# Optimization experiments

Hardware: AMD Instinct MI355X
Metric: run time of the kernel (lower is better)

Reference implementation:

```python
import jax, jax.numpy as jnp
import numpy as np

EMBED = 1024
HEADS = 16
HEAD_DIM = EMBED // HEADS


def setup_inputs() -> dict:
    key = jax.random.key(0)
    ks = jax.random.split(key, 9)
    N, L = 2, 2048
    values = jax.random.normal(ks[0], (N, L, EMBED), dtype=jnp.float32)
    keys = jax.random.normal(ks[1], (N, L, EMBED), dtype=jnp.float32)
    query = jax.random.normal(ks[2], (N, L, EMBED), dtype=jnp.float32)
    mask = jax.random.randint(ks[3], (N, 1, L, L), 0, 2, dtype=jnp.int32)
    s = 1.0 / np.sqrt(HEAD_DIM)
    Wv = jax.random.normal(ks[4], (HEAD_DIM, HEAD_DIM), dtype=jnp.float32) * s
    Wk = jax.random.normal(ks[5], (HEAD_DIM, HEAD_DIM), dtype=jnp.float32) * s
    Wq = jax.random.normal(ks[6], (HEAD_DIM, HEAD_DIM), dtype=jnp.float32) * s
    Wout = jax.random.normal(ks[7], (EMBED, EMBED), dtype=jnp.float32) * (1.0 / np.sqrt(EMBED))
    bout = jax.random.normal(ks[8], (EMBED,), dtype=jnp.float32) * 0.01
    return {"values": values, "keys": keys, "query": query, "mask": mask,
            "Wv": Wv, "Wk": Wk, "Wq": Wq, "Wout": Wout, "bout": bout}


def reference(values, keys, query, mask, Wv, Wk, Wq, Wout, bout):
    N, Lq, _ = query.shape
    Lk = keys.shape[1]
    # split heads: [N, L, H, D]
    v = values.reshape(N, Lk, HEADS, HEAD_DIM)
    k = keys.reshape(N, Lk, HEADS, HEAD_DIM)
    q = query.reshape(N, Lq, HEADS, HEAD_DIM)
    # per-head Linear (weight shared across heads), torch Linear: x @ W.T
    v = jnp.einsum('nlhd,ed->nlhe', v, Wv)
    k = jnp.einsum('nlhd,ed->nlhe', k, Wk)
    q = jnp.einsum('nlhd,ed->nlhe', q, Wq)
    # scores [N, H, Q, K]
    scores = jnp.einsum('nqhd,nkhd->nhqk', q, k)
    scores = jnp.where(mask == 0, jnp.float32(-1e20), scores)
    # NOTE: original scales by sqrt(embed_size), not sqrt(head_dim)
    attn = jax.nn.softmax(scores / jnp.sqrt(jnp.float32(EMBED)), axis=3)
    out = jnp.einsum('nhqk,nkhd->nqhd', attn, v).reshape(N, Lq, EMBED)
    return out @ Wout.T + bout
```

## Files before the change

kernel.cpp:

```cpp
#include <hip/hip_runtime.h>
#include <hip/hip_bf16.h>
#include <stdint.h>

typedef unsigned short u16;
typedef __attribute__((ext_vector_type(8))) short short8;
typedef __attribute__((ext_vector_type(4))) float float4_;

#define N_B   2
#define L_SEQ 2048
#define H_N   16
#define D_H   64
#define EMB   1024
#define KWORDS (L_SEQ/64)

#define C2 0.045084220027780106f

#define KP_OFF 0u
#define VP_OFF (8u*1024u*1024u)
#define X2_OFF (16u*1024u*1024u)
#define MP_OFF (24u*1024u*1024u)
#define WB_OFF (25u*1024u*1024u)

#define PREP_MASK  32768u
#define PREP_CVTW  (PREP_MASK + 512u)
#define PREP_PROJK (PREP_CVTW + 1024u)
#define PREP_TOTAL (PREP_PROJK + 1024u)

__device__ __forceinline__ u16 f2bf(float f) {
    __hip_bfloat16 h = __float2bfloat16(f);
    return *reinterpret_cast<u16*>(&h);
}
__device__ __forceinline__ short8 load8f(const float* p) {
    float4_ a = *(const float4_*)p;
    float4_ b = *(const float4_*)(p + 4);
    short8 r;
    r[0] = (short)f2bf(a[0]); r[1] = (short)f2bf(a[1]);
    r[2] = (short)f2bf(a[2]); r[3] = (short)f2bf(a[3]);
    r[4] = (short)f2bf(b[0]); r[5] = (short)f2bf(b[1]);
    r[6] = (short)f2bf(b[2]); r[7] = (short)f2bf(b[3]);
    return r;
}
__device__ __forceinline__ void gload16(const void* g, void* l) {
    __builtin_amdgcn_global_load_lds(
        (const __attribute__((address_space(1))) uint32_t*)(size_t)g,
        (__attribute__((address_space(3))) uint32_t*)(size_t)l, 16, 0, 0);
}
__device__ __forceinline__ uint32_t cvtpk(float a, float b) {
    uint32_t r;
    asm("v_cvt_pk_bf16_f32 %0, %1, %2" : "=v"(r) : "v"(a), "v"(b));
    return r;
}

__global__ __launch_bounds__(256) void prep_kernel(const int* __restrict__ mask,
                                                   unsigned long long* __restrict__ mp,
                                                   const float* __restrict__ Wout,
                                                   u16* __restrict__ wb,
                                                   const float* __restrict__ keys,
                                                   const float* __restrict__ Wk,
                                                   u16* __restrict__ kp,
                                                   const float* __restrict__ values,
                                                   const float* __restrict__ Wv,
                                                   u16* __restrict__ vpT) {
    unsigned bid = blockIdx.x;
    int tid = threadIdx.x;

    if (bid < PREP_MASK) {
        int wid  = (bid * 256 + tid) >> 6;
        int lane = tid & 63;
        int m = mask[(size_t)wid * 64 + lane];
        unsigned long long bits = __ballot(m != 0);
        if (lane == 0) mp[wid] = bits;
        return;
    }
    if (bid < PREP_CVTW) {
        int i = ((bid - PREP_MASK) * 256 + tid) * 8;
        *(short8*)(wb + i) = load8f(Wout + i);
        return;
    }

    bool isK = bid < PREP_PROJK;
    unsigned lb = bid - (isK ? PREP_CVTW : PREP_PROJK);
    const float* x = isK ? keys : values;
    const float* W = isK ? Wk : Wv;

    int lt = lb & 31;
    int h  = (lb >> 5) & 15;
    int n  = lb >> 9;
    int w = tid >> 6, lane = tid & 63;
    int g = lane >> 4, r16 = lane & 15;
    int l0 = lt * 64 + w * 16;

    const float* xrow = x + ((size_t)(n * L_SEQ + l0 + r16)) * EMB + h * 64;
    short8 a0 = load8f(xrow + 8 * g);
    short8 a1 = load8f(xrow + 32 + 8 * g);

    short8 wf[4][2];
    for (int eb = 0; eb < 4; eb++)
        for (int ch = 0; ch < 2; ch++)
            wf[eb][ch] = load8f(W + (eb * 16 + r16) * 64 + ch * 32 + 8 * g);

    if (isK) {
        u16* ob = kp + ((size_t)((n * H_N + h) * L_SEQ + l0)) * 64;
        for (int eb = 0; eb < 4; eb++) {
            float4_ c = {0.f, 0.f, 0.f, 0.f};
            c = __builtin_amdgcn_mfma_f32_16x16x32_bf16(a0, wf[eb][0], c, 0, 0, 0);
            c = __builtin_amdgcn_mfma_f32_16x16x32_bf16(a1, wf[eb][1], c, 0, 0, 0);
            for (int i = 0; i < 4; i++)
                ob[(size_t)(4 * g + i) * 64 + eb * 16 + r16] = f2bf(c[i]);
        }
    } else {
        u16* obase = vpT + ((size_t)(n * H_N + h)) * (64 * L_SEQ) + l0 + r16;
        for (int eb = 0; eb < 4; eb++) {
            float4_ c = {0.f, 0.f, 0.f, 0.f};
            c = __builtin_amdgcn_mfma_f32_16x16x32_bf16(wf[eb][0], a0, c, 0, 0, 0);
            c = __builtin_amdgcn_mfma_f32_16x16x32_bf16(wf[eb][1], a1, c, 0, 0, 0);
            for (int i = 0; i < 4; i++)
                obase[(size_t)(eb * 16 + 4 * g + i) * L_SEQ] = f2bf(c[i]);
        }
    }
}

__global__ __launch_bounds__(256) void attn_kernel(const float* __restrict__ query,
                                                   const float* __restrict__ Wq,
                                                   const u16* __restrict__ kp,
                                                   const u16* __restrict__ vpT,
                                                   const unsigned long long* __restrict__ mp,
                                                   u16* __restrict__ x2) {
    __shared__ __align__(16) u16 Ks[64 * 64];
    __shared__ __align__(16) u16 Vt[64 * 64];
    __shared__ __align__(16) u16 Pt[4][2][16 * 64];

    int bid = blockIdx.x;
    int nh = bid & 31, qt = bid >> 5;
    int n = nh >> 4;
    int h = nh & 15;
    int tid = threadIdx.x;
    int w = tid >> 6, lane = tid & 63;
    int g = lane >> 4, r16 = lane & 15;
    int q0 = qt * 128 + w * 16;

    const u16* kb  = kp  + ((size_t)nh * L_SEQ) * 64;
    const u16* vtb = vpT + ((size_t)nh) * (64 * L_SEQ);

    int psw = (r16 & 7) << 4;

    short8 wf[4][2];
    for (int eb = 0; eb < 4; eb++)
        for (int ch = 0; ch < 2; ch++)
            wf[eb][ch] = load8f(Wq + (eb * 16 + r16) * 64 + ch * 32 + 8 * g);

    for (int s = 0; s < 2; s++) {
        const float* qrow = query + ((size_t)(n * L_SEQ + q0 + s * 64 + r16)) * EMB + h * 64;
        short8 a0 = load8f(qrow + 8 * g);
        short8 a1 = load8f(qrow + 32 + 8 * g);
        for (int eb = 0; eb < 4; eb++) {
            float4_ c = {0.f, 0.f, 0.f, 0.f};
            c = __builtin_amdgcn_mfma_f32_16x16x32_bf16(a0, wf[eb][0], c, 0, 0, 0);
            c = __builtin_amdgcn_mfma_f32_16x16x32_bf16(a1, wf[eb][1], c, 0, 0, 0);
            for (int i = 0; i < 4; i++) {
                int row = 4 * g + i;
                *(u16*)((char*)Pt[w][s] + row * 128 + (((eb * 16 + r16) * 2) ^ ((row & 7) << 4))) = f2bf(c[i] * C2);
            }
        }
    }
    short8 aq00 = *(const short8*)((char*)Pt[w][0] + r16 * 128 + ((16 * g) ^ psw));
    short8 aq01 = *(const short8*)((char*)Pt[w][0] + r16 * 128 + ((64 + 16 * g) ^ psw));
    short8 aq10 = *(const short8*)((char*)Pt[w][1] + r16 * 128 + ((16 * g) ^ psw));
    short8 aq11 = *(const short8*)((char*)Pt[w][1] + r16 * 128 + ((64 + 16 * g) ^ psw));

    float4_ o0[4] = {}, o1[4] = {};
    float lp0 = 0.f, lp1 = 0.f;
    const unsigned long long* mprow0 = mp + ((size_t)n * L_SEQ + q0 + r16) * KWORDS;
    const unsigned long long* mprow1 = mprow0 + (size_t)64 * KWORDS;

    int rs = (w << 3) + (lane >> 3);
    int cc = (lane & 7) ^ ((lane >> 3) & 7);
    char* ldsK0 = (char*)Ks + w * 1024;
    char* ldsV0 = (char*)Vt + w * 1024;

    for (int kt = 0; kt < 32; kt++) {
        int k0 = kt * 64;
        __syncthreads();
        for (int h2 = 0; h2 < 2; h2++) {
            int r = rs + 32 * h2;
            gload16(kb  + (size_t)(k0 + r) * 64 + cc * 8, ldsK0 + h2 * 4096);
            gload16(vtb + (size_t)r * L_SEQ + k0 + cc * 8, ldsV0 + h2 * 4096);
        }
        __syncthreads();

        unsigned long long word0 = mprow0[kt];
        unsigned long long word1 = mprow1[kt];

        for (int cb = 0; cb < 4; cb++) {
            int row = cb * 16 + r16;
            int sw = (row & 7) << 4;
            short8 bk0 = *(const short8*)((char*)Ks + row * 128 + ((16 * g) ^ sw));
            short8 bk1 = *(const short8*)((char*)Ks + row * 128 + ((64 + 16 * g) ^ sw));
            float4_ c0 = {0.f, 0.f, 0.f, 0.f};
            c0 = __builtin_amdgcn_mfma_f32_16x16x32_bf16(bk0, aq00, c0, 0, 0, 0);
            c0 = __builtin_amdgcn_mfma_f32_16x16x32_bf16(bk1, aq01, c0, 0, 0, 0);
            float4_ c1 = {0.f, 0.f, 0.f, 0.f};
            c1 = __builtin_amdgcn_mfma_f32_16x16x32_bf16(bk0, aq10, c1, 0, 0, 0);
            c1 = __builtin_amdgcn_mfma_f32_16x16x32_bf16(bk1, aq11, c1, 0, 0, 0);

            uint32_t nib0 = (uint32_t)(word0 >> (16 * cb + 4 * g)) & 0xFu;
            uint32_t nib1 = (uint32_t)(word1 >> (16 * cb + 4 * g)) & 0xFu;

            float p0 = (nib0 & 1u) ? exp2f(c0[0]) : 0.f;
            float p1 = (nib0 & 2u) ? exp2f(c0[1]) : 0.f;
            float p2 = (nib0 & 4u) ? exp2f(c0[2]) : 0.f;
            float p3 = (nib0 & 8u) ? exp2f(c0[3]) : 0.f;
            lp0 += (p0 + p1) + (p2 + p3);
            uint2 pk0; pk0.x = cvtpk(p0, p1); pk0.y = cvtpk(p2, p3);
            *(uint2*)((char*)Pt[w][0] + r16 * 128 + ((cb * 32 + 8 * g) ^ psw)) = pk0;

            float q0v = (nib1 & 1u) ? exp2f(c1[0]) : 0.f;
            float q1v = (nib1 & 2u) ? exp2f(c1[1]) : 0.f;
            float q2v = (nib1 & 4u) ? exp2f(c1[2]) : 0.f;
            float q3v = (nib1 & 8u) ? exp2f(c1[3]) : 0.f;
            lp1 += (q0v + q1v) + (q2v + q3v);
            uint2 pk1; pk1.x = cvtpk(q0v, q1v); pk1.y = cvtpk(q2v, q3v);
            *(uint2*)((char*)Pt[w][1] + r16 * 128 + ((cb * 32 + 8 * g) ^ psw)) = pk1;
        }

        short8 pb00 = *(const short8*)((char*)Pt[w][0] + r16 * 128 + ((16 * g) ^ psw));
        short8 pb01 = *(const short8*)((char*)Pt[w][0] + r16 * 128 + ((64 + 16 * g) ^ psw));
        short8 pb10 = *(const short8*)((char*)Pt[w][1] + r16 * 128 + ((16 * g) ^ psw));
        short8 pb11 = *(const short8*)((char*)Pt[w][1] + r16 * 128 + ((64 + 16 * g) ^ psw));

        for (int db = 0; db < 4; db++) {
            int row = db * 16 + r16;
            int sw = (row & 7) << 4;
            short8 av0 = *(const short8*)((char*)Vt + row * 128 + ((16 * g) ^ sw));
            short8 av1 = *(const short8*)((char*)Vt + row * 128 + ((64 + 16 * g) ^ sw));
            o0[db] = __builtin_amdgcn_mfma_f32_16x16x32_bf16(av0, pb00, o0[db], 0, 0, 0);
            o0[db] = __builtin_amdgcn_mfma_f32_16x16x32_bf16(av1, pb01, o0[db], 0, 0, 0);
            o1[db] = __builtin_amdgcn_mfma_f32_16x16x32_bf16(av0, pb10, o1[db], 0, 0, 0);
            o1[db] = __builtin_amdgcn_mfma_f32_16x16x32_bf16(av1, pb11, o1[db], 0, 0, 0);
        }
    }

    float t0 = lp0;
    t0 += __shfl_xor(t0, 16);
    t0 += __shfl_xor(t0, 32);
    float inv0 = 1.f / fmaxf(t0, 1e-30f);
    float t1 = lp1;
    t1 += __shfl_xor(t1, 16);
    t1 += __shfl_xor(t1, 32);
    float inv1 = 1.f / fmaxf(t1, 1e-30f);

    u16* ob0 = x2 + ((size_t)(n * L_SEQ + q0 + r16)) * EMB + h * 64;
    u16* ob1 = x2 + ((size_t)(n * L_SEQ + q0 + 64 + r16)) * EMB + h * 64;
    for (int db = 0; db < 4; db++)
        for (int i = 0; i < 4; i++) {
            ob0[db * 16 + 4 * g + i] = f2bf(o0[db][i] * inv0);
            ob1[db * 16 + 4 * g + i] = f2bf(o1[db][i] * inv1);
        }
}

__global__ __launch_bounds__(512) void outgemm_kernel(const u16* __restrict__ x2,
                                                      const u16* __restrict__ Wb,
                                                      const float* __restrict__ bout,
                                                      float* __restrict__ out) {
    __shared__ __align__(16) u16 As[128 * 64];
    __shared__ __align__(16) u16 Bs[128 * 64];

    int bid = blockIdx.x;
    int mt = bid >> 3, nt = bid & 7;
    int m0 = mt * 128, n0 = nt * 128;
    int tid = threadIdx.x;
    int w = tid >> 6, lane = tid & 63;
    int g = lane >> 4, r16 = lane & 15;
    int wr = w >> 2, wc = w & 3;

    float4_ acc[4][2] = {};

    int rs = (w << 3) + (lane >> 3);
    int cc = (lane & 7) ^ ((lane >> 3) & 7);
    char* ldsA0 = (char*)As + w * 1024;
    char* ldsB0 = (char*)Bs + w * 1024;

    for (int kbk = 0; kbk < 16; kbk++) {
        int kk0 = kbk * 64;
        __syncthreads();
        for (int h2 = 0; h2 < 2; h2++) {
            int r = rs + 64 * h2;
            gload16(x2 + (size_t)(m0 + r) * EMB + kk0 + cc * 8, ldsA0 + h2 * 8192);
            gload16(Wb + (size_t)(n0 + r) * EMB + kk0 + cc * 8, ldsB0 + h2 * 8192);
        }
        __syncthreads();

        short8 afr[4][2], bfr[2][2];
        for (int sm = 0; sm < 4; sm++)
            for (int ch = 0; ch < 2; ch++) {
                int row = wr * 64 + sm * 16 + r16;
                afr[sm][ch] = *(const short8*)((char*)As + row * 128 + ((ch * 64 + 16 * g) ^ ((row & 7) << 4)));
            }
        for (int sn = 0; sn < 2; sn++)
            for (int ch = 0; ch < 2; ch++) {
                int row = wc * 32 + sn * 16 + r16;
                bfr[sn][ch] = *(const short8*)((char*)Bs + row * 128 + ((ch * 64 + 16 * g) ^ ((row & 7) << 4)));
            }
        for (int sm = 0; sm < 4; sm++)
            for (int sn = 0; sn < 2; sn++) {
                acc[sm][sn] = __builtin_amdgcn_mfma_f32_16x16x32_bf16(afr[sm][0], bfr[sn][0], acc[sm][sn], 0, 0, 0);
                acc[sm][sn] = __builtin_amdgcn_mfma_f32_16x16x32_bf16(afr[sm][1], bfr[sn][1], acc[sm][sn], 0, 0, 0);
            }
    }

    for (int sm = 0; sm < 4; sm++)
        for (int sn = 0; sn < 2; sn++) {
            int nn = n0 + wc * 32 + sn * 16 + r16;
            float bv = bout[nn];
            for (int i = 0; i < 4; i++) {
                int mm = m0 + wr * 64 + sm * 16 + 4 * g + i;
                out[(size_t)mm * EMB + nn] = acc[sm][sn][i] + bv;
            }
        }
}

extern "C" void kernel_launch(void* const* d_in, const int* in_sizes, int n_in,
                              void* d_out, int out_size, void* d_ws, size_t ws_size,
                              hipStream_t stream) {
    const float* values = (const float*)d_in[0];
    const float* keys   = (const float*)d_in[1];
    const float* query  = (const float*)d_in[2];
    const int*   mask   = (const int*)d_in[3];
    const float* Wv     = (const float*)d_in[4];
    const float* Wk     = (const float*)d_in[5];
    const float* Wq     = (const float*)d_in[6];
    const float* Wout   = (const float*)d_in[7];
    const float* bout   = (const float*)d_in[8];
    float* out = (float*)d_out;

    char* ws = (char*)d_ws;
    u16* kp  = (u16*)(ws + KP_OFF);
    u16* vpT = (u16*)(ws + VP_OFF);
    u16* x2  = (u16*)(ws + X2_OFF);
    unsigned long long* mpk = (unsigned long long*)(ws + MP_OFF);
    u16* wb  = (u16*)(ws + WB_OFF);

    prep_kernel<<<PREP_TOTAL, 256, 0, stream>>>(mask, mpk, Wout, wb,
                                                keys, Wk, kp, values, Wv, vpT);
    attn_kernel<<<512, 256, 0, stream>>>(query, Wq, kp, vpT, mpk, x2);
    outgemm_kernel<<<256, 512, 0, stream>>>(x2, wb, bout, out);
}
```

Baseline: 252.4 us.

## Double-buffer K/V tiles in attention, halve query tile, coarsen mask packing

```diff
diff --git a/kernel.cpp b/kernel.cpp
--- a/kernel.cpp
+++ b/kernel.cpp
@@ -21,7 +21,7 @@
 #define MP_OFF (24u*1024u*1024u)
 #define WB_OFF (25u*1024u*1024u)
 
-#define PREP_MASK  32768u
+#define PREP_MASK  2048u
 #define PREP_CVTW  (PREP_MASK + 512u)
 #define PREP_PROJK (PREP_CVTW + 1024u)
 #define PREP_TOTAL (PREP_PROJK + 1024u)
@@ -48,6 +48,11 @@
 __device__ __forceinline__ uint32_t cvtpk(float a, float b) {
     uint32_t r;
     asm("v_cvt_pk_bf16_f32 %0, %1, %2" : "=v"(r) : "v"(a), "v"(b));
+    return r;
+}
+__device__ __forceinline__ float fexp2(float x) {
+    float r;
+    asm("v_exp_f32 %0, %1" : "=v"(r) : "v"(x));
     return r;
 }
 
@@ -65,11 +70,14 @@
     int tid = threadIdx.x;
 
     if (bid < PREP_MASK) {
-        int wid  = (bid * 256 + tid) >> 6;
         int lane = tid & 63;
-        int m = mask[(size_t)wid * 64 + lane];
-        unsigned long long bits = __ballot(m != 0);
-        if (lane == 0) mp[wid] = bits;
+        int wv   = tid >> 6;
+        for (int j = 0; j < 16; j++) {
+            int wid = bid * 64 + j * 4 + wv;
+            int m = mask[(size_t)wid * 64 + lane];
+            unsigned long long bits = __ballot(m != 0);
+            if (lane == 0) mp[wid] = bits;
+        }
         return;
     }
     if (bid < PREP_CVTW) {
@@ -126,9 +134,9 @@
                                                    const u16* __restrict__ vpT,
                                                    const unsigned long long* __restrict__ mp,
                                                    u16* __restrict__ x2) {
-    __shared__ __align__(16) u16 Ks[64 * 64];
-    __shared__ __align__(16) u16 Vt[64 * 64];
-    __shared__ __align__(16) u16 Pt[4][2][16 * 64];
+    __shared__ __align__(16) u16 Ks[2][64 * 64];
+    __shared__ __align__(16) u16 Vt[2][64 * 64];
+    __shared__ __align__(16) u16 Pt[4][16 * 64];
 
     int bid = blockIdx.x;
     int nh = bid & 31, qt = bid >> 5;
@@ -137,125 +145,116 @@
     int tid = threadIdx.x;
     int w = tid >> 6, lane = tid & 63;
     int g = lane >> 4, r16 = lane & 15;
-    int q0 = qt * 128 + w * 16;
+    int q0 = qt * 64 + w * 16;
 
     const u16* kb  = kp  + ((size_t)nh * L_SEQ) * 64;
     const u16* vtb = vpT + ((size_t)nh) * (64 * L_SEQ);
 
     int psw = (r16 & 7) << 4;
 
-    short8 wf[4][2];
-    for (int eb = 0; eb < 4; eb++)
-        for (int ch = 0; ch < 2; ch++)
-            wf[eb][ch] = load8f(Wq + (eb * 16 + r16) * 64 + ch * 32 + 8 * g);
-
-    for (int s = 0; s < 2; s++) {
-        const float* qrow = query + ((size_t)(n * L_SEQ + q0 + s * 64 + r16)) * EMB + h * 64;
+    {
+        const float* qrow = query + ((size_t)(n * L_SEQ + q0 + r16)) * EMB + h * 64;
         short8 a0 = load8f(qrow + 8 * g);
         short8 a1 = load8f(qrow + 32 + 8 * g);
         for (int eb = 0; eb < 4; eb++) {
+            short8 w0 = load8f(Wq + (eb * 16 + r16) * 64 + 8 * g);
+            short8 w1 = load8f(Wq + (eb * 16 + r16) * 64 + 32 + 8 * g);
             float4_ c = {0.f, 0.f, 0.f, 0.f};
-            c = __builtin_amdgcn_mfma_f32_16x16x32_bf16(a0, wf[eb][0], c, 0, 0, 0);
-            c = __builtin_amdgcn_mfma_f32_16x16x32_bf16(a1, wf[eb][1], c, 0, 0, 0);
+            c = __builtin_amdgcn_mfma_f32_16x16x32_bf16(a0, w0, c, 0, 0, 0);
+            c = __builtin_amdgcn_mfma_f32_16x16x32_bf16(a1, w1, c, 0, 0, 0);
             for (int i = 0; i < 4; i++) {
                 int row = 4 * g + i;
-                *(u16*)((char*)Pt[w][s] + row * 128 + (((eb * 16 + r16) * 2) ^ ((row & 7) << 4))) = f2bf(c[i] * C2);
-            }
-        }
-    }
-    short8 aq00 = *(const short8*)((char*)Pt[w][0] + r16 * 128 + ((16 * g) ^ psw));
-    short8 aq01 = *(const short8*)((char*)Pt[w][0] + r16 * 128 + ((64 + 16 * g) ^ psw));
-    short8 aq10 = *(const short8*)((char*)Pt[w][1] + r16 * 128 + ((16 * g) ^ psw));
-    short8 aq11 = *(const short8*)((char*)Pt[w][1] + r16 * 128 + ((64 + 16 * g) ^ psw));
-
-    float4_ o0[4] = {}, o1[4] = {};
-    float lp0 = 0.f, lp1 = 0.f;
-    const unsigned long long* mprow0 = mp + ((size_t)n * L_SEQ + q0 + r16) * KWORDS;
-    const unsigned long long* mprow1 = mprow0 + (size_t)64 * KWORDS;
+                *(u16*)((char*)Pt[w] + row * 128 + (((eb * 16 + r16) * 2) ^ ((row & 7) << 4))) = f2bf(c[i] * C2);
+            }
+        }
+    }
+    short8 aq0 = *(const short8*)((char*)Pt[w] + r16 * 128 + ((16 * g) ^ psw));
+    short8 aq1 = *(const short8*)((char*)Pt[w] + r16 * 128 + ((64 + 16 * g) ^ psw));
+
+    float4_ o[4] = {};
+    float lpart = 0.f;
+    const unsigned long long* mprow = mp + ((size_t)n * L_SEQ + q0 + r16) * KWORDS;
 
     int rs = (w << 3) + (lane >> 3);
     int cc = (lane & 7) ^ ((lane >> 3) & 7);
-    char* ldsK0 = (char*)Ks + w * 1024;
-    char* ldsV0 = (char*)Vt + w * 1024;
+
+    #define STAGE(kt_, b_) do {                                                  \
+        int k0_ = (kt_) * 64;                                                    \
+        for (int h2 = 0; h2 < 2; h2++) {                                         \
+            int r_ = rs + 32 * h2;                                               \
+            gload16(kb  + (size_t)(k0_ + r_) * 64 + cc * 8,                      \
+                    (char*)Ks[b_] + w * 1024 + h2 * 4096);                       \
+            gload16(vtb + (size_t)r_ * L_SEQ + k0_ + cc * 8,                     \
+                    (char*)Vt[b_] + w * 1024 + h2 * 4096);                       \
+        }                                                                        \
+    } while (0)
+
+    STAGE(0, 0);
+    int cur = 0;
 
     for (int kt = 0; kt < 32; kt++) {
-        int k0 = kt * 64;
-        __syncthreads();
-        for (int h2 = 0; h2 < 2; h2++) {
-            int r = rs + 32 * h2;
-            gload16(kb  + (size_t)(k0 + r) * 64 + cc * 8, ldsK0 + h2 * 4096);
-            gload16(vtb + (size_t)r * L_SEQ + k0 + cc * 8, ldsV0 + h2 * 4096);
-        }
-        __syncthreads();
-
-        unsigned long long word0 = mprow0[kt];
-        unsigned long long word1 = mprow1[kt];
-
+        if (kt < 31) {
+            STAGE(kt + 1, cur ^ 1);
+            asm volatile("s_waitcnt vmcnt(4)" ::: "memory");
+        } else {
+            asm volatile("s_waitcnt vmcnt(0)" ::: "memory");
+        }
+        __builtin_amdgcn_sched_barrier(0);
+        __builtin_amdgcn_s_barrier();
+        __builtin_amdgcn_sched_barrier(0);
+
+        unsigned long long word = mprow[kt];
+        const char* ksb = (const char*)Ks[cur];
+        const char* vtbuf = (const char*)Vt[cur];
+
+        __builtin_amdgcn_s_setprio(1);
         for (int cb = 0; cb < 4; cb++) {
             int row = cb * 16 + r16;
             int sw = (row & 7) << 4;
-            short8 bk0 = *(const short8*)((char*)Ks + row * 128 + ((16 * g) ^ sw));
-            short8 bk1 = *(const short8*)((char*)Ks + row * 128 + ((64 + 16 * g) ^ sw));
-            float4_ c0 = {0.f, 0.f, 0.f, 0.f};
-            c0 = __builtin_amdgcn_mfma_f32_16x16x32_bf16(bk0, aq00, c0, 0, 0, 0);
-            c0 = __builtin_amdgcn_mfma_f32_16x16x32_bf16(bk1, aq01, c0, 0, 0, 0);
-            float4_ c1 = {0.f, 0.f, 0.f, 0.f};
-            c1 = __builtin_amdgcn_mfma_f32_16x16x32_bf16(bk0, aq10, c1, 0, 0, 0);
-            c1 = __builtin_amdgcn_mfma_f32_16x16x32_bf16(bk1, aq11, c1, 0, 0, 0);
-
-            uint32_t nib0 = (uint32_t)(word0 >> (16 * cb + 4 * g)) & 0xFu;
-            uint32_t nib1 = (uint32_t)(word1 >> (16 * cb + 4 * g)) & 0xFu;
-
-            float p0 = (nib0 & 1u) ? exp2f(c0[0]) : 0.f;
-            float p1 = (nib0 & 2u) ? exp2f(c0[1]) : 0.f;
-            float p2 = (nib0 & 4u) ? exp2f(c0[2]) : 0.f;
-            float p3 = (nib0 & 8u) ? exp2f(c0[3]) : 0.f;
-            lp0 += (p0 + p1) + (p2 + p3);
-            uint2 pk0; pk0.x = cvtpk(p0, p1); pk0.y = cvtpk(p2, p3);
-            *(uint2*)((char*)Pt[w][0] + r16 * 128 + ((cb * 32 + 8 * g) ^ psw)) = pk0;
-
-            float q0v = (nib1 & 1u) ? exp2f(c1[0]) : 0.f;
-            float q1v = (nib1 & 2u) ? exp2f(c1[1]) : 0.f;
-            float q2v = (nib1 & 4u) ? exp2f(c1[2]) : 0.f;
-            float q3v = (nib1 & 8u) ? exp2f(c1[3]) : 0.f;
-            lp1 += (q0v + q1v) + (q2v + q3v);
-            uint2 pk1; pk1.x = cvtpk(q0v, q1v); pk1.y = cvtpk(q2v, q3v);
-            *(uint2*)((char*)Pt[w][1] + r16 * 128 + ((cb * 32 + 8 * g) ^ psw)) = pk1;
-        }
-
-        short8 pb00 = *(const short8*)((char*)Pt[w][0] + r16 * 128 + ((16 * g) ^ psw));
-        short8 pb01 = *(const short8*)((char*)Pt[w][0] + r16 * 128 + ((64 + 16 * g) ^ psw));
-        short8 pb10 = *(const short8*)((char*)Pt[w][1] + r16 * 128 + ((16 * g) ^ psw));
-        short8 pb11 = *(const short8*)((char*)Pt[w][1] + r16 * 128 + ((64 + 16 * g) ^ psw));
+            short8 bk0 = *(const short8*)(ksb + row * 128 + ((16 * g) ^ sw));
+            short8 bk1 = *(const short8*)(ksb + row * 128 + ((64 + 16 * g) ^ sw));
+            float4_ c = {0.f, 0.f, 0.f, 0.f};
+            c = __builtin_amdgcn_mfma_f32_16x16x32_bf16(bk0, aq0, c, 0, 0, 0);
+            c = __builtin_amdgcn_mfma_f32_16x16x32_bf16(bk1, aq1, c, 0, 0, 0);
+
+            uint32_t nib = (uint32_t)(word >> (16 * cb + 4 * g)) & 0xFu;
+            float p0 = (nib & 1u) ? fexp2(c[0]) : 0.f;
+            float p1 = (nib & 2u) ? fexp2(c[1]) : 0.f;
+            float p2 = (nib & 4u) ? fexp2(c[2]) : 0.f;
+            float p3 = (nib & 8u) ? fexp2(c[3]) : 0.f;
+            lpart += (p0 + p1) + (p2 + p3);
+            uint2 pkv; pkv.x = cvtpk(p0, p1); pkv.y = cvtpk(p2, p3);
+            *(uint2*)((char*)Pt[w] + r16 * 128 + ((cb * 32 + 8 * g) ^ psw)) = pkv;
+        }
+
+        short8 pb0 = *(const short8*)((char*)Pt[w] + r16 * 128 + ((16 * g) ^ psw));
+        short8 pb1 = *(const short8*)((char*)Pt[w] + r16 * 128 + ((64 + 16 * g) ^ psw));
 
         for (int db = 0; db < 4; db++) {
             int row = db * 16 + r16;
             int sw = (row & 7) << 4;
-            short8 av0 = *(const short8*)((char*)Vt + row * 128 + ((16 * g) ^ sw));
-            short8 av1 = *(const short8*)((char*)Vt + row * 128 + ((64 + 16 * g) ^ sw));
-            o0[db] = __builtin_amdgcn_mfma_f32_16x16x32_bf16(av0, pb00, o0[db], 0, 0, 0);
-            o0[db] = __builtin_amdgcn_mfma_f32_16x16x32_bf16(av1, pb01, o0[db], 0, 0, 0);
-            o1[db] = __builtin_amdgcn_mfma_f32_16x16x32_bf16(av0, pb10, o1[db], 0, 0, 0);
-            o1[db] = __builtin_amdgcn_mfma_f32_16x16x32_bf16(av1, pb11, o1[db], 0, 0, 0);
-        }
-    }
-
-    float t0 = lp0;
-    t0 += __shfl_xor(t0, 16);
-    t0 += __shfl_xor(t0, 32);
-    float inv0 = 1.f / fmaxf(t0, 1e-30f);
-    float t1 = lp1;
-    t1 += __shfl_xor(t1, 16);
-    t1 += __shfl_xor(t1, 32);
-    float inv1 = 1.f / fmaxf(t1, 1e-30f);
-
-    u16* ob0 = x2 + ((size_t)(n * L_SEQ + q0 + r16)) * EMB + h * 64;
-    u16* ob1 = x2 + ((size_t)(n * L_SEQ + q0 + 64 + r16)) * EMB + h * 64;
+            short8 av0 = *(const short8*)(vtbuf + row * 128 + ((16 * g) ^ sw));
+            short8 av1 = *(const short8*)(vtbuf + row * 128 + ((64 + 16 * g) ^ sw));
+            o[db] = __builtin_amdgcn_mfma_f32_16x16x32_bf16(av0, pb0, o[db], 0, 0, 0);
+            o[db] = __builtin_amdgcn_mfma_f32_16x16x32_bf16(av1, pb1, o[db], 0, 0, 0);
+        }
+        __builtin_amdgcn_s_setprio(0);
+
+        __builtin_amdgcn_sched_barrier(0);
+        __builtin_amdgcn_s_barrier();
+        cur ^= 1;
+    }
+    #undef STAGE
+
+    float tot = lpart;
+    tot += __shfl_xor(tot, 16);
+    tot += __shfl_xor(tot, 32);
+    float inv = 1.f / fmaxf(tot, 1e-30f);
+
+    u16* ob = x2 + ((size_t)(n * L_SEQ + q0 + r16)) * EMB + h * 64;
     for (int db = 0; db < 4; db++)
-        for (int i = 0; i < 4; i++) {
-            ob0[db * 16 + 4 * g + i] = f2bf(o0[db][i] * inv0);
-            ob1[db * 16 + 4 * g + i] = f2bf(o1[db][i] * inv1);
-        }
+        for (int i = 0; i < 4; i++)
+            ob[db * 16 + 4 * g + i] = f2bf(o[db][i] * inv);
 }
 
 __global__ __launch_bounds__(512) void outgemm_kernel(const u16* __restrict__ x2,
@@ -342,6 +341,6 @@
 
     prep_kernel<<<PREP_TOTAL, 256, 0, stream>>>(mask, mpk, Wout, wb,
                                                 keys, Wk, kp, values, Wv, vpT);
-    attn_kernel<<<512, 256, 0, stream>>>(query, Wq, kp, vpT, mpk, x2);
+    attn_kernel<<<1024, 256, 0, stream>>>(query, Wq, kp, vpT, mpk, x2);
     outgemm_kernel<<<256, 512, 0, stream>>>(x2, wb, bout, out);
 }
```

After: 232.6 us. -7.8%, faster.

## Double-buffer LDS tiles in attention and output GEMM, use raw exp2, coarsen mask packing

Applied to the files above, without the earlier changes.

```diff
diff --git a/kernel.cpp b/kernel.cpp
--- a/kernel.cpp
+++ b/kernel.cpp
@@ -21,7 +21,7 @@
 #define MP_OFF (24u*1024u*1024u)
 #define WB_OFF (25u*1024u*1024u)
 
-#define PREP_MASK  32768u
+#define PREP_MASK  2048u
 #define PREP_CVTW  (PREP_MASK + 512u)
 #define PREP_PROJK (PREP_CVTW + 1024u)
 #define PREP_TOTAL (PREP_PROJK + 1024u)
@@ -48,6 +48,11 @@
 __device__ __forceinline__ uint32_t cvtpk(float a, float b) {
     uint32_t r;
     asm("v_cvt_pk_bf16_f32 %0, %1, %2" : "=v"(r) : "v"(a), "v"(b));
+    return r;
+}
+__device__ __forceinline__ float fexp2(float x) {
+    float r;
+    asm("v_exp_f32 %0, %1" : "=v"(r) : "v"(x));
     return r;
 }
 
@@ -65,11 +70,14 @@
     int tid = threadIdx.x;
 
     if (bid < PREP_MASK) {
-        int wid  = (bid * 256 + tid) >> 6;
         int lane = tid & 63;
-        int m = mask[(size_t)wid * 64 + lane];
-        unsigned long long bits = __ballot(m != 0);
-        if (lane == 0) mp[wid] = bits;
+        int wv   = tid >> 6;
+        for (int j = 0; j < 16; j++) {
+            int wid = bid * 64 + j * 4 + wv;
+            int m = mask[(size_t)wid * 64 + lane];
+            unsigned long long bits = __ballot(m != 0);
+            if (lane == 0) mp[wid] = bits;
+        }
         return;
     }
     if (bid < PREP_CVTW) {
@@ -126,8 +134,8 @@
                                                    const u16* __restrict__ vpT,
                                                    const unsigned long long* __restrict__ mp,
                                                    u16* __restrict__ x2) {
-    __shared__ __align__(16) u16 Ks[64 * 64];
-    __shared__ __align__(16) u16 Vt[64 * 64];
+    __shared__ __align__(16) u16 Ks[2][64 * 64];
+    __shared__ __align__(16) u16 Vt[2][64 * 64];
     __shared__ __align__(16) u16 Pt[4][2][16 * 64];
 
     int bid = blockIdx.x;
@@ -143,6 +151,22 @@
     const u16* vtb = vpT + ((size_t)nh) * (64 * L_SEQ);
 
     int psw = (r16 & 7) << 4;
+
+    int rs = (w << 3) + (lane >> 3);
+    int cc = (lane & 7) ^ ((lane >> 3) & 7);
+
+    #define STAGE(kt_, b_) do {                                                  \
+        int k0_ = (kt_) * 64;                                                    \
+        for (int h2 = 0; h2 < 2; h2++) {                                         \
+            int r_ = rs + 32 * h2;                                               \
+            gload16(kb  + (size_t)(k0_ + r_) * 64 + cc * 8,                      \
+                    (char*)Ks[b_] + w * 1024 + h2 * 4096);                       \
+            gload16(vtb + (size_t)r_ * L_SEQ + k0_ + cc * 8,                     \
+                    (char*)Vt[b_] + w * 1024 + h2 * 4096);                       \
+        }                                                                        \
+    } while (0)
+
+    STAGE(0, 0);
 
     short8 wf[4][2];
     for (int eb = 0; eb < 4; eb++)
@@ -173,29 +197,30 @@
     const unsigned long long* mprow0 = mp + ((size_t)n * L_SEQ + q0 + r16) * KWORDS;
     const unsigned long long* mprow1 = mprow0 + (size_t)64 * KWORDS;
 
-    int rs = (w << 3) + (lane >> 3);
-    int cc = (lane & 7) ^ ((lane >> 3) & 7);
-    char* ldsK0 = (char*)Ks + w * 1024;
-    char* ldsV0 = (char*)Vt + w * 1024;
-
+    int cur = 0;
     for (int kt = 0; kt < 32; kt++) {
-        int k0 = kt * 64;
-        __syncthreads();
-        for (int h2 = 0; h2 < 2; h2++) {
-            int r = rs + 32 * h2;
-            gload16(kb  + (size_t)(k0 + r) * 64 + cc * 8, ldsK0 + h2 * 4096);
-            gload16(vtb + (size_t)r * L_SEQ + k0 + cc * 8, ldsV0 + h2 * 4096);
-        }
-        __syncthreads();
-
         unsigned long long word0 = mprow0[kt];
         unsigned long long word1 = mprow1[kt];
-
+        __builtin_amdgcn_sched_barrier(0);
+        if (kt < 31) {
+            STAGE(kt + 1, cur ^ 1);
+            __builtin_amdgcn_sched_barrier(0);
+            asm volatile("s_waitcnt vmcnt(6)" ::: "memory");
+        } else {
+            asm volatile("s_waitcnt vmcnt(0)" ::: "memory");
+        }
+        __builtin_amdgcn_s_barrier();
+        __builtin_amdgcn_sched_barrier(0);
+
+        const char* ksb   = (const char*)Ks[cur];
+        const char* vtbuf = (const char*)Vt[cur];
+
+        __builtin_amdgcn_s_setprio(1);
         for (int cb = 0; cb < 4; cb++) {
             int row = cb * 16 + r16;
             int sw = (row & 7) << 4;
-            short8 bk0 = *(const short8*)((char*)Ks + row * 128 + ((16 * g) ^ sw));
-            short8 bk1 = *(const short8*)((char*)Ks + row * 128 + ((64 + 16 * g) ^ sw));
+            short8 bk0 = *(const short8*)(ksb + row * 128 + ((16 * g) ^ sw));
+            short8 bk1 = *(const short8*)(ksb + row * 128 + ((64 + 16 * g) ^ sw));
             float4_ c0 = {0.f, 0.f, 0.f, 0.f};
             c0 = __builtin_amdgcn_mfma_f32_16x16x32_bf16(bk0, aq00, c0, 0, 0, 0);
             c0 = __builtin_amdgcn_mfma_f32_16x16x32_bf16(bk1, aq01, c0, 0, 0, 0);
@@ -206,18 +231,18 @@
             uint32_t nib0 = (uint32_t)(word0 >> (16 * cb + 4 * g)) & 0xFu;
             uint32_t nib1 = (uint32_t)(word1 >> (16 * cb + 4 * g)) & 0xFu;
 
-            float p0 = (nib0 & 1u) ? exp2f(c0[0]) : 0.f;
-            float p1 = (nib0 & 2u) ? exp2f(c0[1]) : 0.f;
-            float p2 = (nib0 & 4u) ? exp2f(c0[2]) : 0.f;
-            float p3 = (nib0 & 8u) ? exp2f(c0[3]) : 0.f;
+            float p0 = (nib0 & 1u) ? fexp2(c0[0]) : 0.f;
+            float p1 = (nib0 & 2u) ? fexp2(c0[1]) : 0.f;
+            float p2 = (nib0 & 4u) ? fexp2(c0[2]) : 0.f;
+            float p3 = (nib0 & 8u) ? fexp2(c0[3]) : 0.f;
             lp0 += (p0 + p1) + (p2 + p3);
             uint2 pk0; pk0.x = cvtpk(p0, p1); pk0.y = cvtpk(p2, p3);
             *(uint2*)((char*)Pt[w][0] + r16 * 128 + ((cb * 32 + 8 * g) ^ psw)) = pk0;
 
-            float q0v = (nib1 & 1u) ? exp2f(c1[0]) : 0.f;
-            float q1v = (nib1 & 2u) ? exp2f(c1[1]) : 0.f;
-            float q2v = (nib1 & 4u) ? exp2f(c1[2]) : 0.f;
-            float q3v = (nib1 & 8u) ? exp2f(c1[3]) : 0.f;
+            float q0v = (nib1 & 1u) ? fexp2(c1[0]) : 0.f;
+            float q1v = (nib1 & 2u) ? fexp2(c1[1]) : 0.f;
+            float q2v = (nib1 & 4u) ? fexp2(c1[2]) : 0.f;
+            float q3v = (nib1 & 8u) ? fexp2(c1[3]) : 0.f;
             lp1 += (q0v + q1v) + (q2v + q3v);
             uint2 pk1; pk1.x = cvtpk(q0v, q1v); pk1.y = cvtpk(q2v, q3v);
             *(uint2*)((char*)Pt[w][1] + r16 * 128 + ((cb * 32 + 8 * g) ^ psw)) = pk1;
@@ -231,14 +256,20 @@
         for (int db = 0; db < 4; db++) {
             int row = db * 16 + r16;
             int sw = (row & 7) << 4;
-            short8 av0 = *(const short8*)((char*)Vt + row * 128 + ((16 * g) ^ sw));
-            short8 av1 = *(const short8*)((char*)Vt + row * 128 + ((64 + 16 * g) ^ sw));
+            short8 av0 = *(const short8*)(vtbuf + row * 128 + ((16 * g) ^ sw));
+            short8 av1 = *(const short8*)(vtbuf + row * 128 + ((64 + 16 * g) ^ sw));
             o0[db] = __builtin_amdgcn_mfma_f32_16x16x32_bf16(av0, pb00, o0[db], 0, 0, 0);
             o0[db] = __builtin_amdgcn_mfma_f32_16x16x32_bf16(av1, pb01, o0[db], 0, 0, 0);
             o1[db] = __builtin_amdgcn_mfma_f32_16x16x32_bf16(av0, pb10, o1[db], 0, 0, 0);
             o1[db] = __builtin_amdgcn_mfma_f32_16x16x32_bf16(av1, pb11, o1[db], 0, 0, 0);
         }
-    }
+        __builtin_amdgcn_s_setprio(0);
+
+        __builtin_amdgcn_sched_barrier(0);
+        __builtin_amdgcn_s_barrier();
+        cur ^= 1;
+    }
+    #undef STAGE
 
     float t0 = lp0;
     t0 += __shfl_xor(t0, 16);
@@ -262,8 +293,8 @@
                                                       const u16* __restrict__ Wb,
                                                       const float* __restrict__ bout,
                                                       float* __restrict__ out) {
-    __shared__ __align__(16) u16 As[128 * 64];
-    __shared__ __align__(16) u16 Bs[128 * 64];
+    __shared__ __align__(16) u16 As[2][128 * 64];
+    __shared__ __align__(16) u16 Bs[2][128 * 64];
 
     int bid = blockIdx.x;
     int mt = bid >> 3, nt = bid & 7;
@@ -277,36 +308,59 @@
 
     int rs = (w << 3) + (lane >> 3);
     int cc = (lane & 7) ^ ((lane >> 3) & 7);
-    char* ldsA0 = (char*)As + w * 1024;
-    char* ldsB0 = (char*)Bs + w * 1024;
+
+    #define OSTAGE(kb_, b_) do {                                                 \
+        int kk_ = (kb_) * 64;                                                    \
+        for (int h2 = 0; h2 < 2; h2++) {                                         \
+            int r_ = rs + 64 * h2;                                               \
+            gload16(x2 + (size_t)(m0 + r_) * EMB + kk_ + cc * 8,                 \
+                    (char*)As[b_] + w * 1024 + h2 * 8192);                       \
+            gload16(Wb + (size_t)(n0 + r_) * EMB + kk_ + cc * 8,                 \
+                    (char*)Bs[b_] + w * 1024 + h2 * 8192);                       \
+        }                                                                        \
+    } while (0)
+
+    OSTAGE(0, 0);
+    int cur = 0;
 
     for (int kbk = 0; kbk < 16; kbk++) {
-        int kk0 = kbk * 64;
-        __syncthreads();
-        for (int h2 = 0; h2 < 2; h2++) {
-            int r = rs + 64 * h2;
-            gload16(x2 + (size_t)(m0 + r) * EMB + kk0 + cc * 8, ldsA0 + h2 * 8192);
-            gload16(Wb + (size_t)(n0 + r) * EMB + kk0 + cc * 8, ldsB0 + h2 * 8192);
-        }
-        __syncthreads();
+        if (kbk < 15) {
+            OSTAGE(kbk + 1, cur ^ 1);
+            __builtin_amdgcn_sched_barrier(0);
+            asm volatile("s_waitcnt vmcnt(4)" ::: "memory");
+        } else {
+            asm volatile("s_waitcnt vmcnt(0)" ::: "memory");
+        }
+        __builtin_amdgcn_s_barrier();
+        __builtin_amdgcn_sched_barrier(0);
+
+        const char* pa = (const char*)As[cur];
+        const char* pb = (const char*)Bs[cur];
 
         short8 afr[4][2], bfr[2][2];
         for (int sm = 0; sm < 4; sm++)
             for (int ch = 0; ch < 2; ch++) {
                 int row = wr * 64 + sm * 16 + r16;
-                afr[sm][ch] = *(const short8*)((char*)As + row * 128 + ((ch * 64 + 16 * g) ^ ((row & 7) << 4)));
+                afr[sm][ch] = *(const short8*)(pa + row * 128 + ((ch * 64 + 16 * g) ^ ((row & 7) << 4)));
             }
         for (int sn = 0; sn < 2; sn++)
             for (int ch = 0; ch < 2; ch++) {
                 int row = wc * 32 + sn * 16 + r16;
-                bfr[sn][ch] = *(const short8*)((char*)Bs + row * 128 + ((ch * 64 + 16 * g) ^ ((row & 7) << 4)));
+                bfr[sn][ch] = *(const short8*)(pb + row * 128 + ((ch * 64 + 16 * g) ^ ((row & 7) << 4)));
             }
+        __builtin_amdgcn_s_setprio(1);
         for (int sm = 0; sm < 4; sm++)
             for (int sn = 0; sn < 2; sn++) {
                 acc[sm][sn] = __builtin_amdgcn_mfma_f32_16x16x32_bf16(afr[sm][0], bfr[sn][0], acc[sm][sn], 0, 0, 0);
                 acc[sm][sn] = __builtin_amdgcn_mfma_f32_16x16x32_bf16(afr[sm][1], bfr[sn][1], acc[sm][sn], 0, 0, 0);
             }
-    }
+        __builtin_amdgcn_s_setprio(0);
+
+        __builtin_amdgcn_sched_barrier(0);
+        __builtin_amdgcn_s_barrier();
+        cur ^= 1;
+    }
+    #undef OSTAGE
 
     for (int sm = 0; sm < 4; sm++)
         for (int sn = 0; sn < 2; sn++) {
```

Result: faster. 233.7 us (-7.4%).
